# Kernel tuning notes

Measured on AMD Instinct MI355X. Metric: run time of the kernel, lower is better.

Reference implementation:

```python
import jax, jax.numpy as jnp
import numpy as np

B, C_IN, N_PTS = 16, 4, 4096
N_P, DIM = 32, 256
EPS = 1e-5


def conv1d(x, w, b):
    # 1x1 Conv1d: x (B,C,N), w (O,C), b (O)
    return jnp.einsum('bcn,oc->bon', x, w) + b[None, :, None]


def bn(x, g, be):
    # BatchNorm1d in training mode: batch statistics over (B, N)
    m = jnp.mean(x, axis=(0, 2), keepdims=True)
    v = jnp.var(x, axis=(0, 2), keepdims=True)
    return g[None, :, None] * (x - m) * jax.lax.rsqrt(v + EPS) + be[None, :, None]


def softpool(x, n_p=N_P):
    # x: (B, C, N). For each sorting channel c, take indices of its top n_p
    # points and gather ALL C feature channels at those points.
    _, idx = jax.lax.top_k(x, n_p)            # (B, C_sort, n_p) indices into N
    g = jax.vmap(lambda xb, ib: xb[:, ib])(x, idx)  # (B, C_feat, C_sort, n_p)
    return jnp.transpose(g, (0, 1, 3, 2))     # (B, C_feat, n_p, C_sort)


def _forward(x, w1, b1, g1, be1, w2, b2, g2, be2, w3, b3, g3, be3,
             w8, b8, w9, b9, w4, b4, g4, be4, w5, b5, g5, be5,
             w6, b6, g6, be6, w7, b7):
    h = jax.nn.relu(bn(conv1d(x, w1, b1), g1, be1))      # (B,64,N)
    pointfeat = h
    h = jax.nn.relu(bn(conv1d(h, w2, b2), g2, be2))      # (B,128,N)
    h = bn(conv1d(h, w3, b3), g3, be3)                   # (B,256,N)
    sp = softpool(h)                                     # (B,256,32,256)
    # conv8: Conv2d(256,256,(1,256)) -> (B,256,32)
    y = jnp.einsum('bchw,ocw->boh', sp, w8) + b8[None, :, None]
    # conv9: Conv2d(256,256,(32,1)) -> (B,256)
    y = jnp.einsum('bch,och->bo', y, w9) + b9[None, :]
    glob = jnp.broadcast_to(y[:, :, None], (x.shape[0], DIM, x.shape[2]))
    h = jnp.concatenate([glob, pointfeat], axis=1)       # (B,320,N)
    h = jax.nn.relu(bn(conv1d(h, w4, b4), g4, be4))      # (B,512,N)
    h = jax.nn.relu(bn(conv1d(h, w5, b5), g5, be5))      # (B,256,N)
    h = jax.nn.relu(bn(conv1d(h, w6, b6), g6, be6))      # (B,128,N)
    return jnp.tanh(conv1d(h, w7, b7))                   # (B,3,N)


def setup_inputs() -> dict:
    key = jax.random.key(0)
    ks = iter(jax.random.split(key, 64))
    def p(shape, scale=0.05):
        return (jax.random.normal(next(ks), shape, jnp.float32) * scale)
    inp = {}
    inp['x'] = jax.random.normal(next(ks), (B, C_IN, N_PTS), jnp.float32)
    for name, o, i in [('1', 64, 4), ('2', 128, 64), ('3', 256, 128),
                       ('4', 512, 320), ('5', 256, 512), ('6', 128, 256)]:
        inp['w' + name] = p((o, i))
        inp['b' + name] = p((o,))
        inp['g' + name] = jnp.ones((o,), jnp.float32)
        inp['be' + name] = jnp.zeros((o,), jnp.float32)
    inp['w7'] = p((3, 128)); inp['b7'] = p((3,))
    inp['w8'] = p((DIM, DIM, DIM)); inp['b8'] = p((DIM,))
    inp['w9'] = p((DIM, DIM, N_P)); inp['b9'] = p((DIM,))
    return inp


def reference(x, w1, b1, g1, be1, w2, b2, g2, be2, w3, b3, g3, be3,
              w4, b4, g4, be4, w5, b5, g5, be5, w6, b6, g6, be6,
              w7, b7, w8, b8, w9, b9):
    return _forward(x, w1, b1, g1, be1, w2, b2, g2, be2, w3, b3, g3, be3,
                    w8, b8, w9, b9, w4, b4, g4, be4, w5, b5, g5, be5,
                    w6, b6, g6, be6, w7, b7)
```

## Files before the change

kernel.cpp:

```cpp
#include <hip/hip_runtime.h>
#include <cstdint>
#include <cstddef>

#define NPTS 4096
#define BATCH 16

typedef unsigned int uint32;
typedef unsigned long long u64;
typedef unsigned short u16;

typedef __attribute__((ext_vector_type(8))) short short8;
typedef __attribute__((ext_vector_type(16))) float float16;

__device__ __forceinline__ u16 f2bf(float f) {
  uint32 u = __float_as_uint(f);
  u = (u + 0x7fffu + ((u >> 16) & 1u)) >> 16;
  return (u16)u;
}
__device__ __forceinline__ float bf2f(u16 h) {
  return __uint_as_float(((uint32)h) << 16);
}

__global__ __launch_bounds__(256) void conv_gemm(
    const float* __restrict__ act, const float* __restrict__ wt,
    const float* __restrict__ rowbias, const float* __restrict__ obias,
    const float* __restrict__ inScale, const float* __restrict__ inShift,
    float* __restrict__ out, float* __restrict__ partials, int C, int O)
{
  __shared__ float As[16][68];
  __shared__ float Ws[16][68];
  __shared__ float redS[64][17];
  __shared__ float redQ[64][17];
  const int b  = blockIdx.z;
  const int o0 = blockIdx.y * 64;
  const int n0 = blockIdx.x * 64;
  const int t  = threadIdx.x;
  const int tx = t & 15, ty = t >> 4;
  float acc[4][4] = {};
  const float* actb = act + ((size_t)b * C) * NPTS;

  for (int k0 = 0; k0 < C; k0 += 16) {
    const int r  = ty;
    const int cs = tx * 4;
    const int k  = k0 + r;
    float4 av = make_float4(0.f, 0.f, 0.f, 0.f);
    if (k < C) {
      av = *(const float4*)(actb + (size_t)k * NPTS + n0 + cs);
      if (inScale) {
        const float scv = inScale[k], shv = inShift[k];
        av.x = fmaxf(fmaf(av.x, scv, shv), 0.f);
        av.y = fmaxf(fmaf(av.y, scv, shv), 0.f);
        av.z = fmaxf(fmaf(av.z, scv, shv), 0.f);
        av.w = fmaxf(fmaf(av.w, scv, shv), 0.f);
      }
    }
    *(float4*)&As[r][cs] = av;

    float4 wv = make_float4(0.f, 0.f, 0.f, 0.f);
    if (k < C) {
      const float* wp = wt + (size_t)k * O;
      const int o = o0 + cs;
      if (o + 3 < O) {
        wv = *(const float4*)&wp[o];
      } else {
        float tmp[4] = {0.f, 0.f, 0.f, 0.f};
        for (int j = 0; j < 4; ++j) if (o + j < O) tmp[j] = wp[o + j];
        wv = make_float4(tmp[0], tmp[1], tmp[2], tmp[3]);
      }
    }
    *(float4*)&Ws[r][cs] = wv;
    __syncthreads();

    const int kmax = (C - k0 < 16) ? (C - k0) : 16;
    for (int kk = 0; kk < kmax; ++kk) {
      float4 a = *(float4*)&As[kk][tx * 4];
      float4 w = *(float4*)&Ws[kk][ty * 4];
      acc[0][0] += w.x * a.x; acc[0][1] += w.x * a.y; acc[0][2] += w.x * a.z; acc[0][3] += w.x * a.w;
      acc[1][0] += w.y * a.x; acc[1][1] += w.y * a.y; acc[1][2] += w.y * a.z; acc[1][3] += w.y * a.w;
      acc[2][0] += w.z * a.x; acc[2][1] += w.z * a.y; acc[2][2] += w.z * a.z; acc[2][3] += w.z * a.w;
      acc[3][0] += w.w * a.x; acc[3][1] += w.w * a.y; acc[3][2] += w.w * a.z; acc[3][3] += w.w * a.w;
    }
    __syncthreads();
  }

  float s[4], q[4];
  for (int i = 0; i < 4; ++i) {
    const int o = o0 + ty * 4 + i;
    s[i] = 0.f; q[i] = 0.f;
    if (o >= O) continue;
    float base = 0.f;
    if (rowbias) base  = rowbias[(size_t)b * O + o];
    if (obias)   base += obias[o];
    float4 v = make_float4(acc[i][0] + base, acc[i][1] + base, acc[i][2] + base, acc[i][3] + base);
    *(float4*)&out[((size_t)b * O + o) * NPTS + n0 + tx * 4] = v;
    s[i] = v.x + v.y + v.z + v.w;
    q[i] = v.x * v.x + v.y * v.y + v.z * v.z + v.w * v.w;
  }

  if (partials) {
    for (int i = 0; i < 4; ++i) { redS[ty * 4 + i][tx] = s[i]; redQ[ty * 4 + i][tx] = q[i]; }
    __syncthreads();
    if (t < 64) {
      float a = 0.f;
      for (int j = 0; j < 16; ++j) a += redS[t][j];
      partials[((size_t)b * O + o0 + t) * 64 + blockIdx.x] = a;
    } else if (t < 128) {
      float a = 0.f;
      for (int j = 0; j < 16; ++j) a += redQ[t - 64][j];
      partials[(size_t)BATCH * O * 64 + ((size_t)b * O + o0 + t - 64) * 64 + blockIdx.x] = a;
    }
  }
}


__global__ __launch_bounds__(256) void conv1_f64(const float* __restrict__ x,
                                                 const float* __restrict__ w1,
                                                 float* __restrict__ h1f,
                                                 double* __restrict__ psd) {
  const int c = blockIdx.x, b = blockIdx.y;
  const double wa = (double)w1[c * 4 + 0], wb = (double)w1[c * 4 + 1];
  const double wc = (double)w1[c * 4 + 2], wd = (double)w1[c * 4 + 3];
  const float* xb = x + (size_t)b * 4 * NPTS;
  float* dst = h1f + ((size_t)b * 64 + c) * NPTS;
  double s = 0.0, q = 0.0;
  for (int n = threadIdx.x; n < NPTS; n += 256) {
    double v = wa * (double)xb[n] + wb * (double)xb[NPTS + n]
             + wc * (double)xb[2 * NPTS + n] + wd * (double)xb[3 * NPTS + n];
    dst[n] = (float)v;
    s += v; q += v * v;
  }
  __shared__ double ls[4], lq[4];
  for (int off = 32; off; off >>= 1) { s += __shfl_down(s, off, 64); q += __shfl_down(q, off, 64); }
  const int wid = threadIdx.x >> 6;
  if ((threadIdx.x & 63) == 0) { ls[wid] = s; lq[wid] = q; }
  __syncthreads();
  if (threadIdx.x == 0) {
    s = ls[0] + ls[1] + ls[2] + ls[3];
    q = lq[0] + lq[1] + lq[2] + lq[3];
    psd[(size_t)c * 16 + b] = s;
    psd[(size_t)64 * 16 + (size_t)c * 16 + b] = q;
  }
}

__global__ __launch_bounds__(256) void bn_finalize_f64(const double* __restrict__ psd,
                                                       const float* __restrict__ g,
                                                       const float* __restrict__ be,
                                                       double* __restrict__ scd, double* __restrict__ shd,
                                                       float* __restrict__ scf, float* __restrict__ shf,
                                                       int NT) {
  const int c = blockIdx.x;
  const int t = threadIdx.x;
  const double* p2 = psd + (size_t)gridDim.x * NT;
  const int k = (NT + 255) / 256;
  double s = 0.0, q = 0.0;
  for (int i = t * k; i < (t + 1) * k && i < NT; ++i) {
    s += psd[(size_t)c * NT + i];
    q += p2[(size_t)c * NT + i];
  }
  __shared__ double ss[256], qq[256];
  ss[t] = s; qq[t] = q;
  __syncthreads();
  if (t == 0) {
    double S = 0.0, Q = 0.0;
    for (int i = 0; i < 256; ++i) { S += ss[i]; Q += qq[i]; }
    const double m   = S * (1.0 / 65536.0);
    const double var = Q * (1.0 / 65536.0) - m * m;
    const double sc  = (double)g[c] / sqrt(var + 1e-5);
    const double sh  = (double)be[c] - m * sc;
    if (scd) { scd[c] = sc; shd[c] = sh; }
    scf[c] = (float)sc;
    shf[c] = (float)sh;
  }
}

__global__ __launch_bounds__(256) void pack_wtf64(const float* __restrict__ src,
                                                  double* __restrict__ dst,
                                                  int O, int C) {
  int i = blockIdx.x * 256 + threadIdx.x;
  if (i >= O * C) return;
  int c = i / O, o = i - c * O;
  dst[(size_t)c * O + o] = (double)src[(size_t)o * C + c];
}

__global__ __launch_bounds__(256) void conv2_f64v(
    const float* __restrict__ x, const float* __restrict__ w1,
    const double* __restrict__ w2t,
    const double* __restrict__ scd1, const double* __restrict__ shd1,
    double* __restrict__ h2d, float* __restrict__ h2f, double* __restrict__ psd)
{
  __shared__ double Bs[64][65];
  __shared__ double Ws[16][132];
  const int nb = blockIdx.x, b = blockIdx.y;
  const int n0 = nb * 64;
  const int t = threadIdx.x;
  const float* xb = x + (size_t)b * 4 * NPTS + n0;
  for (int i = t; i < 64 * 64; i += 256) {
    const int c1 = i >> 6, n = i & 63;
    double v = (double)w1[c1 * 4 + 0] * (double)xb[n]
             + (double)w1[c1 * 4 + 1] * (double)xb[NPTS + n]
             + (double)w1[c1 * 4 + 2] * (double)xb[2 * NPTS + n]
             + (double)w1[c1 * 4 + 3] * (double)xb[3 * NPTS + n];
    v = v * scd1[c1] + shd1[c1];
    Bs[c1][n] = v > 0.0 ? v : 0.0;
  }
  const int tx = t & 15, ty = t >> 4;
  double acc[8][4] = {};
  for (int ch = 0; ch < 4; ++ch) {
    __syncthreads();
    {
      const int r = t >> 4, oo = (t & 15) * 8;
      const double* srcw = w2t + (size_t)(ch * 16 + r) * 128 + oo;
#pragma unroll
      for (int j = 0; j < 8; ++j) Ws[r][oo + j] = srcw[j];
    }
    __syncthreads();
#pragma unroll
    for (int kk = 0; kk < 16; ++kk) {
      double a[8], bv[4];
#pragma unroll
      for (int j = 0; j < 8; ++j) a[j] = Ws[kk][ty * 8 + j];
#pragma unroll
      for (int j = 0; j < 4; ++j) bv[j] = Bs[ch * 16 + kk][tx + 16 * j];
#pragma unroll
      for (int i = 0; i < 8; ++i)
#pragma unroll
        for (int j = 0; j < 4; ++j) acc[i][j] = fma(a[i], bv[j], acc[i][j]);
    }
  }
  const size_t hb = (size_t)b * 128 * NPTS;
#pragma unroll
  for (int i = 0; i < 8; ++i) {
    const int o = ty * 8 + i;
    double s = 0.0, q = 0.0;
#pragma unroll
    for (int j = 0; j < 4; ++j) {
      const double v = acc[i][j];
      h2d[hb + (size_t)o * NPTS + n0 + tx + 16 * j] = v;
      h2f[hb + (size_t)o * NPTS + n0 + tx + 16 * j] = (float)v;
      s += v; q += v * v;
    }
#pragma unroll
    for (int m = 1; m < 16; m <<= 1) { s += __shfl_xor(s, m, 64); q += __shfl_xor(q, m, 64); }
    if (tx == 0) {
      psd[(size_t)o * 1024 + b * 64 + nb] = s;
      psd[(size_t)128 * 1024 + (size_t)o * 1024 + b * 64 + nb] = q;
    }
  }
}

__global__ __launch_bounds__(256) void pack_wmfma(const float* __restrict__ src,
                                                  u16* __restrict__ ph, u16* __restrict__ pl,
                                                  int O, int Ctot, int cOff, int Csub) {
  int i = blockIdx.x * 256 + threadIdx.x;
  if (i >= O * Csub) return;
  const int KS = Csub >> 4;
  int j    = i & 7;
  int lj   = (i >> 3) & 63;
  int mtks = i >> 9;
  int ks   = mtks % KS;
  int mt   = mtks / KS;
  int o = mt * 32 + (lj & 31);
  int c = ks * 16 + (lj >> 5) * 8 + j;
  float v = src[(size_t)o * Ctot + cOff + c];
  u16 h = f2bf(v);
  ph[i] = h;
  pl[i] = f2bf(v - bf2f(h));
}

__global__ __launch_bounds__(256) void conv_mfma(
    const float* __restrict__ act, const u16* __restrict__ wh, const u16* __restrict__ wl,
    const float* __restrict__ rowbias,
    const float* __restrict__ inScale, const float* __restrict__ inShift,
    float* __restrict__ out, float* __restrict__ ps, int C, int O)
{
  __shared__ u16 Bh[2][4096];
  __shared__ u16 Bl[2][4096];
  const int b  = blockIdx.z;
  const int o0 = blockIdx.y * 128;
  const int n0 = blockIdx.x * 128;
  const int t  = threadIdx.x;
  const int l  = t & 63, wva = t >> 6;
  const int mt = blockIdx.y * 4 + wva;
  const int KS = C >> 4;
  const int NCH = C >> 5;
  const float* actb = act + ((size_t)b * C) * NPTS;

  float16 acc[4];
#pragma unroll
  for (int ns = 0; ns < 4; ++ns)
#pragma unroll
    for (int r = 0; r < 16; ++r) acc[ns][r] = 0.f;

  const int cq = t >> 5;
  const int nq = t & 31;
  const int nn = n0 + nq * 4;
  const int ksl = cq >> 2, oct = (cq >> 1) & 1, j0 = (cq & 1) * 4;

  float va[4][4];
  float4 scv = make_float4(1.f,1.f,1.f,1.f), shv = make_float4(0.f,0.f,0.f,0.f);

  auto loadChunk = [&](int ch) {
    const int cb = ch * 32 + cq * 4;
#pragma unroll
    for (int i2 = 0; i2 < 4; ++i2) {
      float4 v4 = *(const float4*)(actb + (size_t)(cb + i2) * NPTS + nn);
      va[i2][0] = v4.x; va[i2][1] = v4.y; va[i2][2] = v4.z; va[i2][3] = v4.w;
    }
    if (inScale) {
      scv = *(const float4*)&inScale[cb];
      shv = *(const float4*)&inShift[cb];
    }
  };
  auto applyBN = [&]() {
    if (!inScale) return;
#pragma unroll
    for (int d = 0; d < 4; ++d) {
      va[0][d] = fmaxf(fmaf(va[0][d], scv.x, shv.x), 0.f);
      va[1][d] = fmaxf(fmaf(va[1][d], scv.y, shv.y), 0.f);
      va[2][d] = fmaxf(fmaf(va[2][d], scv.z, shv.z), 0.f);
      va[3][d] = fmaxf(fmaf(va[3][d], scv.w, shv.w), 0.f);
    }
  };
  auto convWrite = [&](int buf) {
#pragma unroll
    for (int d = 0; d < 4; ++d) {
      const int nrel = nq * 4 + d;
      const int ns = nrel >> 5, li = nrel & 31;
      u16 h0 = f2bf(va[0][d]), h1 = f2bf(va[1][d]), h2 = f2bf(va[2][d]), h3 = f2bf(va[3][d]);
      u16 q0 = f2bf(va[0][d] - bf2f(h0));
      u16 q1 = f2bf(va[1][d] - bf2f(h1));
      u16 q2 = f2bf(va[2][d] - bf2f(h2));
      u16 q3 = f2bf(va[3][d] - bf2f(h3));
      const int idx = ((ksl * 4 + ns) * 64 + oct * 32 + li) * 8 + j0;
      *(ushort4*)&Bh[buf][idx] = make_ushort4(h0, h1, h2, h3);
      *(ushort4*)&Bl[buf][idx] = make_ushort4(q0, q1, q2, q3);
    }
  };

  loadChunk(0);
  applyBN();
  convWrite(0);
  __syncthreads();

  for (int ch = 0; ch < NCH; ++ch) {
    const size_t abase = (((size_t)mt * KS + ch * 2) * 64 + (size_t)l) * 8;
    short8 AH0 = *(const short8*)(wh + abase);
    short8 AH1 = *(const short8*)(wh + abase + 512);
    short8 AL0 = *(const short8*)(wl + abase);
    short8 AL1 = *(const short8*)(wl + abase + 512);
    const bool more = (ch + 1 < NCH);
    if (more) loadChunk(ch + 1);

    const u16* bh = Bh[ch & 1];
    const u16* bl = Bl[ch & 1];
#pragma unroll
    for (int ns = 0; ns < 4; ++ns) {
      short8 BH0 = *(const short8*)&bh[((0 * 4 + ns) * 64 + l) * 8];
      short8 BL0 = *(const short8*)&bl[((0 * 4 + ns) * 64 + l) * 8];
      acc[ns] = __builtin_amdgcn_mfma_f32_32x32x16_bf16(AL0, BH0, acc[ns], 0, 0, 0);
      acc[ns] = __builtin_amdgcn_mfma_f32_32x32x16_bf16(AH0, BL0, acc[ns], 0, 0, 0);
      acc[ns] = __builtin_amdgcn_mfma_f32_32x32x16_bf16(AH0, BH0, acc[ns], 0, 0, 0);
      short8 BH1 = *(const short8*)&bh[((4 + ns) * 64 + l) * 8];
      short8 BL1 = *(const short8*)&bl[((4 + ns) * 64 + l) * 8];
      acc[ns] = __builtin_amdgcn_mfma_f32_32x32x16_bf16(AL1, BH1, acc[ns], 0, 0, 0);
      acc[ns] = __builtin_amdgcn_mfma_f32_32x32x16_bf16(AH1, BL1, acc[ns], 0, 0, 0);
      acc[ns] = __builtin_amdgcn_mfma_f32_32x32x16_bf16(AH1, BH1, acc[ns], 0, 0, 0);
    }
    if (more) { applyBN(); convWrite((ch + 1) & 1); }
    __syncthreads();
  }

  const int col = l & 31, half = l >> 5;
  float sv[16], sq[16];
#pragma unroll
  for (int r = 0; r < 16; ++r) {
    const int o = o0 + wva * 32 + (r & 3) + 8 * (r >> 2) + 4 * half;
    const float base = rowbias ? rowbias[(size_t)b * O + o] : 0.f;
    float s = 0.f, q = 0.f;
#pragma unroll
    for (int ns = 0; ns < 4; ++ns) {
      float val = acc[ns][r] + base;
      out[((size_t)b * O + o) * NPTS + n0 + ns * 32 + col] = val;
      s += val; q += val * val;
    }
    sv[r] = s; sq[r] = q;
  }
  if (ps) {
#pragma unroll
    for (int r = 0; r < 16; ++r) {
#pragma unroll
      for (int m = 1; m < 32; m <<= 1) {
        sv[r] += __shfl_xor(sv[r], m, 64);
        sq[r] += __shfl_xor(sq[r], m, 64);
      }
    }
    if (col == 0) {
#pragma unroll
      for (int r = 0; r < 16; ++r) {
        const int o = o0 + wva * 32 + (r & 3) + 8 * (r >> 2) + 4 * half;
        ps[((size_t)b * O + o) * 32 + blockIdx.x] = sv[r];
        ps[(size_t)BATCH * O * 32 + ((size_t)b * O + o) * 32 + blockIdx.x] = sq[r];
      }
    }
  }
}

__global__ __launch_bounds__(256) void bn_finalize(const float* __restrict__ ps,
                                                   const float* __restrict__ g, const float* __restrict__ be,
                                                   float* __restrict__ scale, float* __restrict__ shift,
                                                   int O, int NT) {
  const int c = blockIdx.x;
  const int total = BATCH * NT;
  const float* p2 = ps + (size_t)BATCH * O * NT;
  const int t = threadIdx.x;
  float s = 0.f, q = 0.f;
  for (int e = t; e < total; e += 256) {
    const int b = e / NT, nt = e - b * NT;
    const size_t a = ((size_t)b * O + c) * NT + nt;
    s += ps[a];
    q += p2[a];
  }
#pragma unroll
  for (int m = 32; m; m >>= 1) {
    s += __shfl_down(s, m, 64);
    q += __shfl_down(q, m, 64);
  }
  __shared__ float lsS[4], lsQ[4];
  const int wid = t >> 6;
  if ((t & 63) == 0) { lsS[wid] = s; lsQ[wid] = q; }
  __syncthreads();
  if (t == 0) {
    s = lsS[0] + lsS[1] + lsS[2] + lsS[3];
    q = lsQ[0] + lsQ[1] + lsQ[2] + lsQ[3];
    const float inv = 1.f / 65536.f;
    float m   = s * inv;
    float var = q * inv - m * m;
    float sc  = g[c] * rsqrtf(var + 1e-5f);
    scale[c] = sc;
    shift[c] = be[c] - m * sc;
  }
}

#define NCAND 40
__global__ __launch_bounds__(256) void topk40_f32(const float* __restrict__ h3,
                                                  int* __restrict__ cand) {
  __shared__ u64 wl[4][NCAND];
  const int c = blockIdx.x, b = blockIdx.y;
  const float* src = h3 + ((size_t)b * 256 + c) * NPTS;
  const int t = threadIdx.x;
  const int l = t & 63, w = t >> 6;
  const int base = w * 1024;

  uint32 k[16];
  uint32 bk = 0;
#pragma unroll
  for (int s = 0; s < 16; ++s) {
    uint32 u = __float_as_uint(src[base + s * 64 + l]);
    uint32 m32 = ((int)u < 0) ? ~u : (u | 0x80000000u);
    k[s] = m32;
    bk = m32 > bk ? m32 : bk;
  }

  for (int r = 0; r < NCAND; ++r) {
    uint32 m = bk;
#pragma unroll
    for (int off = 1; off < 64; off <<= 1) {
      uint32 o = (uint32)__shfl_xor((int)m, off, 64);
      m = o > m ? o : m;
    }
    const u64 mask = __ballot(bk == m);
    const int owner = (int)(__ffsll((unsigned long long)mask) - 1);
    if (l == owner) {
      bool done = false;
      int ri = 0;
#pragma unroll
      for (int s = 0; s < 16; ++s) {
        if (!done && k[s] == m) { ri = base + s * 64 + l; k[s] = 0; done = true; }
      }
      wl[w][r] = ((u64)m << 32) | (u64)(4095 - ri);
      uint32 m0 = k[0]  > k[1]  ? k[0]  : k[1];
      uint32 m1 = k[2]  > k[3]  ? k[2]  : k[3];
      uint32 m2 = k[4]  > k[5]  ? k[4]  : k[5];
      uint32 m3 = k[6]  > k[7]  ? k[6]  : k[7];
      uint32 m4 = k[8]  > k[9]  ? k[8]  : k[9];
      uint32 m5 = k[10] > k[11] ? k[10] : k[11];
      uint32 m6 = k[12] > k[13] ? k[12] : k[13];
      uint32 m7 = k[14] > k[15] ? k[14] : k[15];
      m0 = m0 > m1 ? m0 : m1;  m2 = m2 > m3 ? m2 : m3;
      m4 = m4 > m5 ? m4 : m5;  m6 = m6 > m7 ? m6 : m7;
      m0 = m0 > m2 ? m0 : m2;  m4 = m4 > m6 ? m4 : m6;
      bk = m0 > m4 ? m0 : m4;
    }
  }
  __syncthreads();

  if (t < 4) {
    int* dst = cand + ((size_t)b * 256 + c) * NCAND;
    int cp = 0;
    u64 cv = wl[t][0];
    for (int r = 0; r < NCAND; ++r) {
      u64 mv = cv;
      u64 ov;
      ov = __shfl_xor((unsigned long long)mv, 1, 64); if (ov > mv) mv = ov;
      ov = __shfl_xor((unsigned long long)mv, 2, 64); if (ov > mv) mv = ov;
      if (t == 0) dst[r] = 4095 - (int)(mv & 0xFFFu);
      if (mv == cv) {
        ++cp;
        cv = (cp < NCAND) ? wl[t][cp] : 0;
      }
    }
  }
}

__global__ __launch_bounds__(256) void transpose_h2(const double* __restrict__ h2d,
                                                    double* __restrict__ h2T) {
  __shared__ double tile[32][33];
  const int b = blockIdx.z;
  const int n0 = blockIdx.x * 32, c0 = blockIdx.y * 32;
  const int tx = threadIdx.x & 31, ty = threadIdx.x >> 5;
  const double* src = h2d + (size_t)b * 128 * NPTS;
  for (int j = 0; j < 4; ++j)
    tile[ty + j * 8][tx] = src[(size_t)(c0 + ty + j * 8) * NPTS + n0 + tx];
  __syncthreads();
  double* dst = h2T + (size_t)b * NPTS * 128;
  for (int j = 0; j < 4; ++j)
    dst[(size_t)(n0 + ty + j * 8) * 128 + c0 + tx] = tile[tx][ty + j * 8];
}

__global__ __launch_bounds__(64) void rerank_f64(const double* __restrict__ h2T,
                                                 const float* __restrict__ w3,
                                                 const double* __restrict__ scd2,
                                                 const double* __restrict__ shd2,
                                                 const int* __restrict__ cand,
                                                 int* __restrict__ idxp) {
  __shared__ u64 keys[NCAND];
  const int o = blockIdx.x, b = blockIdx.y;
  const int l = threadIdx.x;
  const double wA = (double)w3[(size_t)o * 128 + l];
  const double wB = (double)w3[(size_t)o * 128 + l + 64];
  const double sA = scd2[l],      hA = shd2[l];
  const double sB = scd2[l + 64], hB = shd2[l + 64];
  const int* cd = cand + ((size_t)b * 256 + o) * NCAND;
  const double* hb = h2T + (size_t)b * NPTS * 128;
  for (int kk = 0; kk < NCAND; ++kk) {
    const int n = cd[kk];
    const double* col = hb + (size_t)n * 128;
    double va = col[l] * sA + hA;       va = va > 0.0 ? va : 0.0;
    double vb = col[l + 64] * sB + hB;  vb = vb > 0.0 ? vb : 0.0;
    double p = wA * va + wB * vb;
#pragma unroll
    for (int off = 32; off; off >>= 1) p += __shfl_down(p, off, 64);
    if (l == 0) {
      u64 u = (u64)__double_as_longlong(p);
      u64 m = ((long long)u < 0) ? ~u : (u | 0x8000000000000000ULL);
      m = (m & ~0xFFFULL) | (u64)(4095 - n);
      keys[kk] = m;
    }
  }
  __syncthreads();
  u64 kv = (l < NCAND) ? keys[l] : 0;
  int* dst = idxp + ((size_t)b * 256 + o) * 32;
  for (int r = 0; r < 32; ++r) {
    u64 m = kv;
#pragma unroll
    for (int off = 1; off < 64; off <<= 1) {
      u64 o2 = __shfl_xor((unsigned long long)m, off, 64);
      if (o2 > m) m = o2;
    }
    if (l == 0) dst[r] = 4095 - (int)(m & 0xFFFULL);
    if (m == kv) kv = 0;
  }
}

__global__ __launch_bounds__(256) void transpose_h3f(const float* __restrict__ h3,
                                                     float* __restrict__ h3T,
                                                     const float* __restrict__ sc,
                                                     const float* __restrict__ sh) {
  __shared__ float tile[32][33];
  const int b = blockIdx.z;
  const int n0 = blockIdx.x * 32, c0 = blockIdx.y * 32;
  const int tx = threadIdx.x & 31, ty = threadIdx.x >> 5;
  const float* src = h3 + (size_t)b * 256 * NPTS;
  for (int j = 0; j < 4; ++j)
    tile[ty + j * 8][tx] = src[(size_t)(c0 + ty + j * 8) * NPTS + n0 + tx];
  __syncthreads();
  float* dst = h3T + (size_t)b * NPTS * 256;
  const float scv = sc[c0 + tx], shv = sh[c0 + tx];
  for (int j = 0; j < 4; ++j)
    dst[(size_t)(n0 + ty + j * 8) * 256 + c0 + tx] = fmaf(tile[tx][ty + j * 8], scv, shv);
}

__global__ __launch_bounds__(256) void transpack_w8(const float* __restrict__ w8,
                                                    u16* __restrict__ w8h, u16* __restrict__ w8l) {
  __shared__ float tile[64][65];
  const int m0 = blockIdx.x * 64, w0 = blockIdx.y * 64;
  const int tx = threadIdx.x & 63, ty = threadIdx.x >> 6;
#pragma unroll
  for (int j = 0; j < 16; ++j)
    tile[ty + j * 4][tx] = w8[(size_t)(m0 + ty + j * 4) * 256 + w0 + tx];
  __syncthreads();
  const int m = m0 + tx;
  const int o = m >> 8, c = m & 255;
  const int mt = (o >> 5) & 7;
  const int lane = (o & 31) + ((c >> 3) & 1) * 32;
  const int ks = (c >> 4) & 15;
  const int jj = c & 7;
#pragma unroll
  for (int j = 0; j < 16; ++j) {
    const int w = w0 + ty + j * 4;
    float v = tile[tx][ty + j * 4];
    size_t f = ((((size_t)w * 8 + mt) * 16 + ks) * 64 + lane) * 8 + jj;
    u16 h = f2bf(v);
    w8h[f] = h;
    w8l[f] = f2bf(v - bf2f(h));
  }
}

#define Y8N (BATCH * 256 * 32)
__global__ __launch_bounds__(256, 1) void conv8_mfma(
    const float* __restrict__ h3T, const u16* __restrict__ w8h,
    const u16* __restrict__ w8l, const int* __restrict__ idxp,
    float* __restrict__ y8p)
{
  __shared__ u16 G[2][8192];
  const int wg = blockIdx.x;
  const int oq = blockIdx.y;
  const int bg = blockIdx.z;
  const int t  = threadIdx.x;
  const int l  = t & 63, wv = t >> 6;
  const int mt = oq * 4 + wv;

  float16 accH[4], accL[4];
  for (int i = 0; i < 4; ++i)
    for (int r = 0; r < 16; ++r) { accH[i][r] = 0.f; accL[i][r] = 0.f; }

  short8 ah[16], al[16];
  const int hrow  = t >> 3;
  const int cbase = (t & 7) * 32;
  float4 g4[8];

  auto issueG = [&](int step) {
    int wi = step >> 2, bi = step & 3;
    int w = wg * 8 + wi;
    int b = bg * 4 + bi;
    int n = idxp[((size_t)b * 256 + w) * 32 + hrow];
    const float* src = h3T + ((size_t)b * NPTS + n) * 256 + cbase;
#pragma unroll
    for (int j = 0; j < 8; ++j) g4[j] = *(const float4*)&src[j * 4];
  };
  auto writeG = [&](int buf) {
#pragma unroll
    for (int a = 0; a < 4; ++a) {
      int c8 = (cbase >> 3) + a;
      int ks = c8 >> 1;
      int lp = hrow + (c8 & 1) * 32;
      float4 v0 = g4[a * 2], v1 = g4[a * 2 + 1];
      uint32 u0 = (uint32)f2bf(v0.x) | ((uint32)f2bf(v0.y) << 16);
      uint32 u1 = (uint32)f2bf(v0.z) | ((uint32)f2bf(v0.w) << 16);
      uint32 u2 = (uint32)f2bf(v1.x) | ((uint32)f2bf(v1.y) << 16);
      uint32 u3 = (uint32)f2bf(v1.z) | ((uint32)f2bf(v1.w) << 16);
      *(uint4*)&G[buf][((size_t)ks * 64 + lp) * 8] = make_uint4(u0, u1, u2, u3);
    }
  };

  issueG(0); writeG(0);
  __syncthreads();

  for (int wi = 0; wi < 8; ++wi) {
    const int w = wg * 8 + wi;
    {
      const size_t base = (((size_t)w * 8 + mt) * 16) * 512 + (size_t)l * 8;
#pragma unroll
      for (int ks = 0; ks < 16; ++ks) {
        ah[ks] = *(const short8*)(w8h + base + ks * 512);
        al[ks] = *(const short8*)(w8l + base + ks * 512);
      }
    }
#pragma unroll
    for (int bi = 0; bi < 4; ++bi) {
      const int step = wi * 4 + bi;
      const int cur = bi & 1;
      if (step < 31) issueG(step + 1);
      const u16* Gc = G[cur];
#pragma unroll
      for (int ks = 0; ks < 16; ++ks) {
        short8 bf = *(const short8*)&Gc[((size_t)ks * 64 + l) * 8];
        accH[bi] = __builtin_amdgcn_mfma_f32_32x32x16_bf16(ah[ks], bf, accH[bi], 0, 0, 0);
        accL[bi] = __builtin_amdgcn_mfma_f32_32x32x16_bf16(al[ks], bf, accL[bi], 0, 0, 0);
      }
      if (step < 31) writeG(1 - cur);
      __syncthreads();
    }
  }

  const int h = l & 31;
  const int rbase = oq * 128 + wv * 32 + 4 * (l >> 5);
#pragma unroll
  for (int bi = 0; bi < 4; ++bi) {
    int b = bg * 4 + bi;
    float* dst = y8p + ((size_t)(wg * BATCH + b) * 256) * 32;
#pragma unroll
    for (int r = 0; r < 16; ++r) {
      int o = rbase + (r & 3) + 8 * (r >> 2);
      dst[(size_t)o * 32 + h] = accH[bi][r] + accL[bi][r];
    }
  }
}

__global__ __launch_bounds__(256) void y8_reduce(const float* __restrict__ y8p,
                                                 const float* __restrict__ b8,
                                                 float* __restrict__ y8) {
  int i = blockIdx.x * 256 + threadIdx.x;
  float s = b8[(i >> 5) & 255];
#pragma unroll
  for (int p = 0; p < 32; ++p) s += y8p[(size_t)p * Y8N + i];
  y8[i] = s;
}

__global__ __launch_bounds__(256) void conv9_kernel(const float* __restrict__ y8,
                                                    const float* __restrict__ w9,
                                                    const float* __restrict__ b9,
                                                    float* __restrict__ y9) {
  const int o = blockIdx.x, b = blockIdx.y;
  const float* yb = y8 + (size_t)b * 8192;
  const float* wo = w9 + (size_t)o * 8192;
  float s = 0.f;
  for (int i = threadIdx.x * 4; i < 8192; i += 1024) {
    float4 v = *(const float4*)&yb[i];
    float4 u = *(const float4*)&wo[i];
    s += v.x * u.x + v.y * u.y + v.z * u.z + v.w * u.w;
  }
  for (int off = 32; off; off >>= 1) s += __shfl_down(s, off, 64);
  __shared__ float ls[4];
  const int wid = threadIdx.x >> 6;
  if ((threadIdx.x & 63) == 0) ls[wid] = s;
  __syncthreads();
  if (threadIdx.x == 0) y9[(size_t)b * 256 + o] = ls[0] + ls[1] + ls[2] + ls[3] + b9[o];
}

__global__ __launch_bounds__(256) void cvec_kernel(const float* __restrict__ y9,
                                                   const float* __restrict__ w4,
                                                   float* __restrict__ cvec) {
  int tid = blockIdx.x * 256 + threadIdx.x;
  if (tid >= BATCH * 512) return;
  const int b = tid >> 9, o = tid & 511;
  const float* row = w4 + (size_t)o * 320;
  const float* yb  = y9 + (size_t)b * 256;
  float s = 0.f;
  for (int c = 0; c < 256; c += 4) {
    float4 u = *(const float4*)&row[c];
    s += u.x * yb[c] + u.y * yb[c + 1] + u.z * yb[c + 2] + u.w * yb[c + 3];
  }
  cvec[(size_t)b * 512 + o] = s;
}

__global__ __launch_bounds__(256) void transpose_w(const float* __restrict__ src,
                                                   float* __restrict__ dst,
                                                   int O, int Ctot, int cOff, int Csub) {
  int i = blockIdx.x * 256 + threadIdx.x;
  if (i >= O * Csub) return;
  int c = i / O, o = i - c * O;
  dst[(size_t)c * O + o] = src[(size_t)o * Ctot + cOff + c];
}

__global__ __launch_bounds__(256) void tanh_out(const float* __restrict__ raw,
                                                float* __restrict__ out) {
  int i = blockIdx.x * 256 + threadIdx.x;
  if (i < BATCH * 3 * NPTS) out[i] = tanhf(raw[i]);
}

extern "C" void kernel_launch(void* const* d_in, const int* in_sizes, int n_in,
                              void* d_out, int out_size, void* d_ws, size_t ws_size,
                              hipStream_t stream) {
  (void)in_sizes; (void)n_in; (void)ws_size; (void)out_size;
  const float* x   = (const float*)d_in[0];
  const float* w1  = (const float*)d_in[1];
  const float* g1  = (const float*)d_in[3];
  const float* be1 = (const float*)d_in[4];
  const float* w2  = (const float*)d_in[5];
  const float* g2  = (const float*)d_in[7];
  const float* be2 = (const float*)d_in[8];
  const float* w3  = (const float*)d_in[9];
  const float* g3  = (const float*)d_in[11];
  const float* be3 = (const float*)d_in[12];
  const float* w4  = (const float*)d_in[13];
  const float* g4  = (const float*)d_in[15];
  const float* be4 = (const float*)d_in[16];
  const float* w5  = (const float*)d_in[17];
  const float* g5  = (const float*)d_in[19];
  const float* be5 = (const float*)d_in[20];
  const float* w6  = (const float*)d_in[21];
  const float* g6  = (const float*)d_in[23];
  const float* be6 = (const float*)d_in[24];
  const float* w7  = (const float*)d_in[25];
  const float* b7  = (const float*)d_in[26];
  const float* w8  = (const float*)d_in[27];
  const float* b8  = (const float*)d_in[28];
  const float* w9  = (const float*)d_in[29];
  const float* b9  = (const float*)d_in[30];

  char* ws = (char*)d_ws;
  size_t off = 0;
  auto alloc = [&](size_t bytes) -> void* {
    void* p = ws + off;
    off += (bytes + 255) & ~(size_t)255;
    return p;
  };
  float* Q1  = (float*)alloc((size_t)BATCH * 64  * NPTS * 4);
  float* Q2  = (float*)alloc((size_t)BATCH * 128 * NPTS * 4);
  float* Q3  = (float*)alloc((size_t)BATCH * 256 * NPTS * 4);
  float* Q4  = (float*)alloc((size_t)BATCH * 256 * NPTS * 4);
  float* Q5  = (float*)alloc((size_t)BATCH * 256 * NPTS * 4);
  int*   idx  = (int*)alloc((size_t)BATCH * 256 * 32 * 4);
  int*   cand = (int*)alloc((size_t)BATCH * 256 * NCAND * 4);
  float* y8   = (float*)alloc((size_t)Y8N * 4);
  float* y9   = (float*)alloc((size_t)BATCH * 256 * 4);
  float* cvec = (float*)alloc((size_t)BATCH * 512 * 4);
  float* ps   = (float*)alloc((size_t)2 * BATCH * 512 * 32 * 4);
  double* psd = (double*)alloc((size_t)2 * 256 * 1024 * 8);
  float* scb  = (float*)alloc((size_t)6 * 1024 * 4);
  double* scdb = (double*)alloc((size_t)1024 * 8);
  float* w7t  = (float*)alloc(128 * 3 * 4);
  u16* ph3 = (u16*)alloc(256 * 128 * 2);  u16* pl3 = (u16*)alloc(256 * 128 * 2);
  u16* ph4 = (u16*)alloc(512 * 64  * 2);  u16* pl4 = (u16*)alloc(512 * 64  * 2);
  u16* ph5 = (u16*)alloc(256 * 512 * 2);  u16* pl5 = (u16*)alloc(256 * 512 * 2);
  u16* ph6 = (u16*)alloc(128 * 256 * 2);  u16* pl6 = (u16*)alloc(128 * 256 * 2);
  double* w2t = (double*)alloc((size_t)64 * 128 * 8);

  double* h2d = (double*)Q3;
  float*  h2f = (float*)Q5;
  double* h2T = (double*)Q5;
  float*  h3f = Q4;
  u16*   w8h = (u16*)Q4;
  u16*   w8l = (u16*)Q4 + (size_t)16777216;
  float* y8p = Q2;
  float* h4  = Q2;
  float* h5  = Q5;
  float* h6  = Q2;

  float* sc[6]; float* sh[6];
  for (int i = 0; i < 6; ++i) { sc[i] = scb + i * 1024; sh[i] = scb + i * 1024 + 512; }
  double* scd1 = scdb;        double* shd1 = scdb + 64;
  double* scd2 = scdb + 128;  double* shd2 = scdb + 256;

  transpose_w<<<(128 * 3 + 255) / 256, 256, 0, stream>>>(w7, w7t, 3, 128, 0, 128);
  pack_wmfma<<<(256 * 128 + 255) / 256, 256, 0, stream>>>(w3, ph3, pl3, 256, 128, 0,   128);
  pack_wmfma<<<(512 * 64  + 255) / 256, 256, 0, stream>>>(w4, ph4, pl4, 512, 320, 256, 64);
  pack_wmfma<<<(256 * 512 + 255) / 256, 256, 0, stream>>>(w5, ph5, pl5, 256, 512, 0,   512);
  pack_wmfma<<<(128 * 256 + 255) / 256, 256, 0, stream>>>(w6, ph6, pl6, 128, 256, 0,   256);
  pack_wtf64<<<(128 * 64 + 255) / 256,  256, 0, stream>>>(w2, w2t, 128, 64);

  conv1_f64<<<dim3(64, BATCH), 256, 0, stream>>>(x, w1, Q1, psd);
  bn_finalize_f64<<<64, 256, 0, stream>>>(psd, g1, be1, scd1, shd1, sc[0], sh[0], 16);
  conv2_f64v<<<dim3(64, BATCH), 256, 0, stream>>>(x, w1, w2t, scd1, shd1, h2d, h2f, psd);
  bn_finalize_f64<<<128, 256, 0, stream>>>(psd, g2, be2, scd2, shd2, sc[1], sh[1], 1024);
  conv_mfma<<<dim3(32, 2, BATCH), 256, 0, stream>>>(h2f, ph3, pl3, nullptr, sc[1], sh[1], h3f, ps, 128, 256);
  bn_finalize<<<256, 256, 0, stream>>>(ps, g3, be3, sc[2], sh[2], 256, 32);

  topk40_f32<<<dim3(256, BATCH), 256, 0, stream>>>(h3f, cand);
  transpose_h2<<<dim3(NPTS / 32, 4, BATCH), 256, 0, stream>>>(h2d, h2T);
  rerank_f64<<<dim3(256, BATCH), 64, 0, stream>>>(h2T, w3, scd2, shd2, cand, idx);
  transpose_h3f<<<dim3(NPTS / 32, 8, BATCH), 256, 0, stream>>>(h3f, Q3, sc[2], sh[2]);

  transpack_w8<<<dim3(1024, 4), 256, 0, stream>>>(w8, w8h, w8l);

  conv8_mfma<<<dim3(32, 2, 4), 256, 0, stream>>>(Q3, w8h, w8l, idx, y8p);
  y8_reduce<<<Y8N / 256, 256, 0, stream>>>(y8p, b8, y8);
  conv9_kernel<<<dim3(256, BATCH), 256, 0, stream>>>(y8, w9, b9, y9);
  cvec_kernel<<<(BATCH * 512 + 255) / 256, 256, 0, stream>>>(y9, w4, cvec);

  conv_mfma<<<dim3(32, 4, BATCH), 256, 0, stream>>>(Q1, ph4, pl4, cvec, sc[0], sh[0], h4, ps, 64, 512);
  bn_finalize<<<512, 256, 0, stream>>>(ps, g4, be4, sc[3], sh[3], 512, 32);
  conv_mfma<<<dim3(32, 2, BATCH), 256, 0, stream>>>(h4, ph5, pl5, nullptr, sc[3], sh[3], h5, ps, 512, 256);
  bn_finalize<<<256, 256, 0, stream>>>(ps, g5, be5, sc[4], sh[4], 256, 32);
  conv_mfma<<<dim3(32, 1, BATCH), 256, 0, stream>>>(h5, ph6, pl6, nullptr, sc[4], sh[4], h6, ps, 256, 128);
  bn_finalize<<<128, 256, 0, stream>>>(ps, g6, be6, sc[5], sh[5], 128, 32);
  conv_gemm<<<dim3(64, 1, BATCH), 256, 0, stream>>>(h6, w7t, nullptr, b7, sc[5], sh[5], Q1, nullptr, 128, 3);
  tanh_out<<<(BATCH * 3 * NPTS) / 256, 256, 0, stream>>>(Q1, (float*)d_out);
}
```

Baseline: 856.3 us.

## Sort per-thread top-k keys in registers and use a DPP wave max

Each thread now sorts its 16 keys with an in-register bitonic network, after packing the point's local index into the low 10 bits of the key. Each of the 40 selection rounds then takes a DPP-based wave max over one register (the thread's current top). The winning thread shifts its sorted list down, replacing the shuffle-xor reduction, ballot and 16-way rescan that ran every round. The cost is that the low 10 mantissa bits of each key are lost, so values that differ only in those bits can be ordered wrongly among the candidates.

```diff
diff --git a/kernel.cpp b/kernel.cpp
--- a/kernel.cpp
+++ b/kernel.cpp
@@ -441,6 +441,16 @@
   }
 }
 
+__device__ __forceinline__ int wave_max_i32(int v) {
+  v = max(v, __builtin_amdgcn_update_dpp(v, v, 0x111, 0xf, 0xf, false));
+  v = max(v, __builtin_amdgcn_update_dpp(v, v, 0x112, 0xf, 0xf, false));
+  v = max(v, __builtin_amdgcn_update_dpp(v, v, 0x114, 0xf, 0xf, false));
+  v = max(v, __builtin_amdgcn_update_dpp(v, v, 0x118, 0xf, 0xf, false));
+  v = max(v, __builtin_amdgcn_update_dpp(v, v, 0x142, 0xa, 0xf, false));
+  v = max(v, __builtin_amdgcn_update_dpp(v, v, 0x143, 0xc, 0xf, false));
+  return __builtin_amdgcn_readlane(v, 63);
+}
+
 #define NCAND 40
 __global__ __launch_bounds__(256) void topk40_f32(const float* __restrict__ h3,
                                                   int* __restrict__ cand) {
@@ -451,45 +461,44 @@
   const int l = t & 63, w = t >> 6;
   const int base = w * 1024;
 
-  uint32 k[16];
-  uint32 bk = 0;
+  int k[16];
 #pragma unroll
   for (int s = 0; s < 16; ++s) {
-    uint32 u = __float_as_uint(src[base + s * 64 + l]);
+    const int loc = s * 64 + l;
+    uint32 u = __float_as_uint(src[base + loc]);
     uint32 m32 = ((int)u < 0) ? ~u : (u | 0x80000000u);
-    k[s] = m32;
-    bk = m32 > bk ? m32 : bk;
+    uint32 packed = (m32 & ~0x3FFu) | (uint32)(1023 - loc);
+    k[s] = (int)(packed ^ 0x80000000u);
+  }
+
+#pragma unroll
+  for (int kk = 2; kk <= 16; kk <<= 1) {
+#pragma unroll
+    for (int j = kk >> 1; j > 0; j >>= 1) {
+#pragma unroll
+      for (int i = 0; i < 16; ++i) {
+        const int ij = i ^ j;
+        if (ij > i) {
+          const bool up = ((i & kk) == 0);
+          const int a = k[i], bb = k[ij];
+          const bool sw = up ? (a > bb) : (a < bb);
+          k[i]  = sw ? bb : a;
+          k[ij] = sw ? a : bb;
+        }
+      }
+    }
   }
 
   for (int r = 0; r < NCAND; ++r) {
-    uint32 m = bk;
-#pragma unroll
-    for (int off = 1; off < 64; off <<= 1) {
-      uint32 o = (uint32)__shfl_xor((int)m, off, 64);
-      m = o > m ? o : m;
-    }
-    const u64 mask = __ballot(bk == m);
-    const int owner = (int)(__ffsll((unsigned long long)mask) - 1);
-    if (l == owner) {
-      bool done = false;
-      int ri = 0;
-#pragma unroll
-      for (int s = 0; s < 16; ++s) {
-        if (!done && k[s] == m) { ri = base + s * 64 + l; k[s] = 0; done = true; }
-      }
-      wl[w][r] = ((u64)m << 32) | (u64)(4095 - ri);
-      uint32 m0 = k[0]  > k[1]  ? k[0]  : k[1];
-      uint32 m1 = k[2]  > k[3]  ? k[2]  : k[3];
-      uint32 m2 = k[4]  > k[5]  ? k[4]  : k[5];
-      uint32 m3 = k[6]  > k[7]  ? k[6]  : k[7];
-      uint32 m4 = k[8]  > k[9]  ? k[8]  : k[9];
-      uint32 m5 = k[10] > k[11] ? k[10] : k[11];
-      uint32 m6 = k[12] > k[13] ? k[12] : k[13];
-      uint32 m7 = k[14] > k[15] ? k[14] : k[15];
-      m0 = m0 > m1 ? m0 : m1;  m2 = m2 > m3 ? m2 : m3;
-      m4 = m4 > m5 ? m4 : m5;  m6 = m6 > m7 ? m6 : m7;
-      m0 = m0 > m2 ? m0 : m2;  m4 = m4 > m6 ? m4 : m6;
-      bk = m0 > m4 ? m0 : m4;
+    const int m = wave_max_i32(k[15]);
+    if (k[15] == m) {
+      const uint32 m32 = (uint32)m ^ 0x80000000u;
+      const int loc = 1023 - (int)(m32 & 0x3FFu);
+      const int ri = base + loc;
+      wl[w][r] = ((u64)m32 << 32) | (u64)(4095 - ri);
+#pragma unroll
+      for (int s = 15; s > 0; --s) k[s] = k[s - 1];
+      k[0] = (int)0x80000000;
     }
   }
   __syncthreads();
```

New measurement: 787.3 us (median of 2 runs). -8.1%, faster.
